# Kernel optimization log

Measured on AMD Instinct MI355X. Metric: run time of the kernel, lower is better.

## Reference

```python
import jax, jax.numpy as jnp
import numpy as np

N_NODES = 10000
N_EDGES = 160000
D = 256
L = 2
EPS = 1e-5


def setup_inputs() -> dict:
    key = jax.random.key(0)
    ks = jax.random.split(key, 12)
    s = 0.05  # weight init scale to keep activations tame
    return {
        "node_h": jax.random.normal(ks[0], (N_NODES, D), jnp.float32),
        "edge_h": jax.random.normal(ks[1], (N_EDGES, D), jnp.float32),
        "src": jax.random.randint(ks[2], (N_EDGES,), 0, N_NODES, jnp.int32),
        "dst": jax.random.randint(ks[3], (N_EDGES,), 0, N_NODES, jnp.int32),
        "Kw": jax.random.normal(ks[4], (L, 2 * D, D), jnp.float32) * s,
        "Kb": jnp.zeros((L, D), jnp.float32),
        "Vw": jax.random.normal(ks[5], (L, 2 * D, D), jnp.float32) * s,
        "Vb": jnp.zeros((L, D), jnp.float32),
        "Qw": jax.random.normal(ks[6], (L, D, D), jnp.float32) * s,
        "Qb": jnp.zeros((L, D), jnp.float32),
        "Ww": jax.random.normal(ks[7], (L, 2 * D, D), jnp.float32) * s,
        "Wb": jnp.zeros((L, D), jnp.float32),
        "Ew": jax.random.normal(ks[8], (L, 3 * D, D), jnp.float32) * s,
        "Eb": jnp.zeros((L, D), jnp.float32),
        "ln_g": jnp.ones((D,), jnp.float32),
        "ln_b": jnp.zeros((D,), jnp.float32),
    }


def _layernorm(x, g, b):
    mu = jnp.mean(x, axis=-1, keepdims=True)
    var = jnp.mean(jnp.square(x - mu), axis=-1, keepdims=True)
    return (x - mu) * jax.lax.rsqrt(var + EPS) * g + b


def _hypergraph_layer(h_n, h_e, src, dst, Kw, Kb, Vw, Vb, Qw, Qb, Ww, Wb, Ew, Eb):
    n = h_n.shape[0]
    src_h = h_n[src]                                   # [E, D] gather
    msg = jnp.concatenate([src_h * h_e, src_h], axis=1)  # [E, 2D]
    Q = h_n @ Qw + Qb                                  # [N, D]
    K = msg @ Kw + Kb                                  # [E, D]
    V = msg @ Vw + Vb                                  # [E, D]
    alpha = Q[dst] * K                                 # v_mul_e -> [E, D]
    # edge_softmax: per-destination-node, per-feature softmax over edges
    m = jax.ops.segment_max(alpha, dst, num_segments=n)
    e = jnp.exp(alpha - m[dst])
    z = jax.ops.segment_sum(e, dst, num_segments=n)
    a = e / z[dst]
    agg = jax.ops.segment_sum(a * V, dst, num_segments=n)  # sum aggregation [N, D]
    h_n_new = jnp.concatenate([agg, h_n], axis=1) @ Ww + Wb
    h_e_new = jnp.concatenate([h_n_new[src], h_n_new[dst], h_e], axis=1) @ Ew + Eb
    return h_n_new, h_e_new


def reference(node_h, edge_h, src, dst, Kw, Kb, Vw, Vb, Qw, Qb, Ww, Wb, Ew, Eb, ln_g, ln_b):
    h_n, h_e = node_h, edge_h
    for l in range(L):  # small fixed layer count
        h_n, h_e = _hypergraph_layer(h_n, h_e, src, dst,
                                     Kw[l], Kb[l], Vw[l], Vb[l], Qw[l], Qb[l],
                                     Ww[l], Wb[l], Ew[l], Eb[l])
        # relu -> layernorm; dropout is identity in eval mode
        h_n = _layernorm(jax.nn.relu(h_n), ln_g, ln_b)
        h_e = _layernorm(jax.nn.relu(h_e), ln_g, ln_b)
    return h_n, h_e
```

## Files before the change

kernel.cpp:

```cpp
#include <hip/hip_runtime.h>

#define NN 10000
#define NE 160000
#define DD 256
#define LEPS 1e-5f

typedef __attribute__((ext_vector_type(8))) short short8v;
typedef __attribute__((ext_vector_type(4))) float floatx4;
typedef unsigned short US;

static __device__ __forceinline__ US f2bf(float f){
  unsigned u = __builtin_bit_cast(unsigned, f);
  u += 0x7FFFu + ((u >> 16) & 1u);
  return (US)(u >> 16);
}
static __device__ __forceinline__ float bf2f(US s){
  unsigned u = ((unsigned)s) << 16;
  return __builtin_bit_cast(float, u);
}

__global__ void pack_k(const float* __restrict__ B, US* __restrict__ Bp, int Krows){
  int i = blockIdx.x * blockDim.x + threadIdx.x;
  int tot = (Krows >> 3) << 8;
  if (i >= tot) return;
  int kb = i >> 8, n = i & 255;
  union { US h[8]; uint4 q; } pk;
#pragma unroll
  for (int j = 0; j < 8; ++j) pk.h[j] = f2bf(B[(size_t)(kb*8 + j)*DD + n]);
  *(uint4*)(Bp + (size_t)i * 8) = pk.q;
}

template<int MODE, int LNM>
__global__ __launch_bounds__(256, 2)
void gemm_k(const float* __restrict__ p0, const float* __restrict__ p1,
            const int* __restrict__ idx0, const int* __restrict__ idx1,
            const US* __restrict__ Bp, const float* __restrict__ bias,
            const float* __restrict__ lg, const float* __restrict__ lb,
            float* __restrict__ Craw, float* __restrict__ Cln, int M, int K)
{
  __shared__ __align__(16) US Alds[64][40];
  __shared__ __align__(16) US Blds[4 * 256 * 8];
  __shared__ float S1[4][64], S2[4][64];
  const int tid  = threadIdx.x;
  const int lane = tid & 63;
  const int wav  = tid >> 6;
  const int bm   = blockIdx.x * 64;

  floatx4 acc[4][4];
#pragma unroll
  for (int i = 0; i < 4; ++i)
#pragma unroll
    for (int j = 0; j < 4; ++j) acc[i][j] = (floatx4){0.f,0.f,0.f,0.f};

  const int ar = tid >> 2;
  const int ak = (tid & 3) << 3;
  int grow = bm + ar; if (grow > M - 1) grow = M - 1;

  const float* rA = nullptr; const float* rB = nullptr; const float* rC = nullptr;
  if (MODE == 0) { rA = p0 + (size_t)grow * DD; }
  else if (MODE == 2) { rA = p0 + (size_t)grow * DD; rB = p1 + (size_t)grow * DD; }
  else { int s0 = idx0[grow], s1 = idx1[grow];
         rA = p0 + (size_t)s0 * DD; rB = p0 + (size_t)s1 * DD; rC = p1 + (size_t)grow * DD; }

  const int rq = lane >> 4;
  const int cl = lane & 15;

  for (int k0 = 0; k0 < K; k0 += 32) {
    const int kk = k0 + ak;
    float4 x0, x1;
    if (MODE == 0) {
      x0 = *(const float4*)(rA + kk); x1 = *(const float4*)(rA + kk + 4);
    } else if (MODE == 2) {
      const float* s = (kk < DD) ? (rA + kk) : (rB + kk - DD);
      x0 = *(const float4*)s; x1 = *(const float4*)(s + 4);
    } else {
      const float* s = (kk < DD) ? (rA + kk) : (kk < 2*DD ? (rB + kk - DD) : (rC + kk - 2*DD));
      x0 = *(const float4*)s; x1 = *(const float4*)(s + 4);
    }
    union { US h[8]; uint4 q; } pk;
    pk.h[0]=f2bf(x0.x); pk.h[1]=f2bf(x0.y); pk.h[2]=f2bf(x0.z); pk.h[3]=f2bf(x0.w);
    pk.h[4]=f2bf(x1.x); pk.h[5]=f2bf(x1.y); pk.h[6]=f2bf(x1.z); pk.h[7]=f2bf(x1.w);
    *(uint4*)&Alds[ar][ak] = pk.q;

    const uint4* bsrc = (const uint4*)(Bp + (size_t)(k0 >> 3) * 2048);
    uint4* bdst = (uint4*)Blds;
#pragma unroll
    for (int t = 0; t < 4; ++t) bdst[tid + t*256] = bsrc[tid + t*256];
    __syncthreads();

    short8v af[4], bfr[4];
#pragma unroll
    for (int i = 0; i < 4; ++i) af[i] = *(const short8v*)&Alds[i*16 + cl][rq*8];
#pragma unroll
    for (int j = 0; j < 4; ++j) bfr[j] = *(const short8v*)&Blds[(size_t)(rq*256 + wav*64 + j*16 + cl) * 8];
#pragma unroll
    for (int i = 0; i < 4; ++i)
#pragma unroll
      for (int j = 0; j < 4; ++j)
        acc[i][j] = __builtin_amdgcn_mfma_f32_16x16x32_bf16(af[i], bfr[j], acc[i][j], 0, 0, 0);
    __syncthreads();
  }

  if constexpr (LNM == 0) {
#pragma unroll
    for (int i = 0; i < 4; ++i)
#pragma unroll
      for (int r = 0; r < 4; ++r) {
        int gm = bm + i*16 + rq*4 + r;
        if (gm < M) {
#pragma unroll
          for (int j = 0; j < 4; ++j) {
            int n = wav*64 + j*16 + cl;
            Craw[(size_t)gm*DD + n] = acc[i][j][r] + bias[n];
          }
        }
      }
  } else {
#pragma unroll
    for (int i = 0; i < 4; ++i)
#pragma unroll
      for (int j = 0; j < 4; ++j) {
        int n = wav*64 + j*16 + cl;
        float bs = bias[n];
#pragma unroll
        for (int r = 0; r < 4; ++r) {
          int gm = bm + i*16 + rq*4 + r;
          float val = acc[i][j][r] + bs;
          if constexpr (LNM == 2) { if (gm < M) Craw[(size_t)gm*DD + n] = val; }
          acc[i][j][r] = fmaxf(val, 0.f);
        }
      }
#pragma unroll
    for (int i = 0; i < 4; ++i)
#pragma unroll
      for (int r = 0; r < 4; ++r) {
        float s1 = 0.f, s2 = 0.f;
#pragma unroll
        for (int j = 0; j < 4; ++j){ float v = acc[i][j][r]; s1 += v; s2 += v*v; }
#pragma unroll
        for (int o = 1; o < 16; o <<= 1){ s1 += __shfl_xor(s1, o, 64); s2 += __shfl_xor(s2, o, 64); }
        if (cl == 0){ S1[wav][i*16 + rq*4 + r] = s1; S2[wav][i*16 + rq*4 + r] = s2; }
      }
    __syncthreads();
#pragma unroll
    for (int i = 0; i < 4; ++i)
#pragma unroll
      for (int r = 0; r < 4; ++r) {
        int rr = i*16 + rq*4 + r;
        float t1 = S1[0][rr] + S1[1][rr] + S1[2][rr] + S1[3][rr];
        float t2 = S2[0][rr] + S2[1][rr] + S2[2][rr] + S2[3][rr];
        float mu = t1 * (1.f/256.f);
        float var = t2 * (1.f/256.f) - mu*mu;
        float rs = rsqrtf(fmaxf(var, 0.f) + LEPS);
        int gm = bm + i*16 + rq*4 + r;
        if (gm < M) {
#pragma unroll
          for (int j = 0; j < 4; ++j) {
            int n = wav*64 + j*16 + cl;
            Cln[(size_t)gm*DD + n] = (acc[i][j][r] - mu) * rs * lg[n] + lb[n];
          }
        }
      }
  }
}

__global__ __launch_bounds__(256, 2)
void gemm_kv_k(const float* __restrict__ p0, const float* __restrict__ p1,
               const int* __restrict__ idx0,
               const US* __restrict__ BpK, const US* __restrict__ BpV,
               const float* __restrict__ biasK, const float* __restrict__ biasV,
               const int* __restrict__ eperm,
               US* __restrict__ Km, US* __restrict__ Vm, int M, int K)
{
  __shared__ __align__(16) US Alds[64][40];
  __shared__ __align__(16) US BldsK[4 * 256 * 8];
  __shared__ __align__(16) US BldsV[4 * 256 * 8];
  const int tid  = threadIdx.x;
  const int lane = tid & 63;
  const int wav  = tid >> 6;
  const int bm   = blockIdx.x * 64;

  floatx4 accK[4][4], accV[4][4];
#pragma unroll
  for (int i = 0; i < 4; ++i)
#pragma unroll
    for (int j = 0; j < 4; ++j){ accK[i][j] = (floatx4){0.f,0.f,0.f,0.f}; accV[i][j] = (floatx4){0.f,0.f,0.f,0.f}; }

  const int ar = tid >> 2;
  const int ak = (tid & 3) << 3;
  int grow = bm + ar; if (grow > M - 1) grow = M - 1;
  int s = idx0[grow];
  const float* rA = p0 + (size_t)s * DD;
  const float* rB = p1 + (size_t)grow * DD;

  const int rq = lane >> 4;
  const int cl = lane & 15;

  for (int k0 = 0; k0 < K; k0 += 32) {
    const int kk = k0 + ak;
    float4 x0, x1;
    if (kk < DD) {
      x0 = *(const float4*)(rA + kk); x1 = *(const float4*)(rA + kk + 4);
      float4 m0 = *(const float4*)(rB + kk), m1 = *(const float4*)(rB + kk + 4);
      x0.x*=m0.x; x0.y*=m0.y; x0.z*=m0.z; x0.w*=m0.w;
      x1.x*=m1.x; x1.y*=m1.y; x1.z*=m1.z; x1.w*=m1.w;
    } else {
      x0 = *(const float4*)(rA + kk - DD); x1 = *(const float4*)(rA + kk - DD + 4);
    }
    union { US h[8]; uint4 q; } pk;
    pk.h[0]=f2bf(x0.x); pk.h[1]=f2bf(x0.y); pk.h[2]=f2bf(x0.z); pk.h[3]=f2bf(x0.w);
    pk.h[4]=f2bf(x1.x); pk.h[5]=f2bf(x1.y); pk.h[6]=f2bf(x1.z); pk.h[7]=f2bf(x1.w);
    *(uint4*)&Alds[ar][ak] = pk.q;

    const uint4* bsK = (const uint4*)(BpK + (size_t)(k0 >> 3) * 2048);
    const uint4* bsV = (const uint4*)(BpV + (size_t)(k0 >> 3) * 2048);
    uint4* bdK = (uint4*)BldsK; uint4* bdV = (uint4*)BldsV;
#pragma unroll
    for (int t = 0; t < 4; ++t){ bdK[tid + t*256] = bsK[tid + t*256]; bdV[tid + t*256] = bsV[tid + t*256]; }
    __syncthreads();

    short8v af[4], bK[4], bV[4];
#pragma unroll
    for (int i = 0; i < 4; ++i) af[i] = *(const short8v*)&Alds[i*16 + cl][rq*8];
#pragma unroll
    for (int j = 0; j < 4; ++j){
      size_t bi = (size_t)(rq*256 + wav*64 + j*16 + cl) * 8;
      bK[j] = *(const short8v*)&BldsK[bi];
      bV[j] = *(const short8v*)&BldsV[bi];
    }
#pragma unroll
    for (int i = 0; i < 4; ++i)
#pragma unroll
      for (int j = 0; j < 4; ++j){
        accK[i][j] = __builtin_amdgcn_mfma_f32_16x16x32_bf16(af[i], bK[j], accK[i][j], 0, 0, 0);
        accV[i][j] = __builtin_amdgcn_mfma_f32_16x16x32_bf16(af[i], bV[j], accV[i][j], 0, 0, 0);
      }
    __syncthreads();
  }

#pragma unroll
  for (int i = 0; i < 4; ++i)
#pragma unroll
    for (int r = 0; r < 4; ++r) {
      int gm = bm + i*16 + rq*4 + r;
      if (gm < M) {
        int pg = eperm[gm];
#pragma unroll
        for (int j = 0; j < 4; ++j) {
          int n = wav*64 + j*16 + cl;
          Km[(size_t)pg*DD + n] = f2bf(accK[i][j][r] + biasK[n]);
          Vm[(size_t)pg*DD + n] = f2bf(accV[i][j][r] + biasV[n]);
        }
      }
    }
}

__global__ void count_k(const int* __restrict__ dst, int* __restrict__ cnt, int e){
  int i = blockIdx.x * blockDim.x + threadIdx.x;
  if (i < e) atomicAdd(&cnt[dst[i]], 1);
}
__global__ void scan_k(const int* __restrict__ cnt, int* __restrict__ rp, int n){
  __shared__ int part[256];
  const int t = threadIdx.x;
  const int chunk = (n + 255) / 256;
  int lo = t * chunk, hi = lo + chunk; if (hi > n) hi = n; if (lo > n) lo = n;
  int s = 0;
  for (int i = lo; i < hi; ++i) s += cnt[i];
  part[t] = s; __syncthreads();
  if (t == 0){ int run = 0; for (int i = 0; i < 256; ++i){ int tmp = part[i]; part[i] = run; run += tmp; } rp[n] = run; }
  __syncthreads();
  int run = part[t];
  for (int i = lo; i < hi; ++i){ rp[i] = run; run += cnt[i]; }
}
__global__ void scatter_k(const int* __restrict__ dst, const int* __restrict__ rp,
                          int* __restrict__ pos, int* __restrict__ eperm, int e){
  int i = blockIdx.x * blockDim.x + threadIdx.x;
  if (i >= e) return;
  int d = dst[i];
  int p = atomicAdd(&pos[d], 1);
  eperm[i] = rp[d] + p;
}

__global__ __launch_bounds__(256)
void node_agg_k(const int* __restrict__ rp,
                const float* __restrict__ Q, const US* __restrict__ Km,
                const US* __restrict__ Vm, float* __restrict__ agg)
{
  int d = blockIdx.x, f = threadIdx.x;
  int beg = rp[d], end = rp[d + 1];
  float q = Q[(size_t)d * DD + f];
  float m = -3.0e38f, z = 0.f, s = 0.f;
  for (int i = beg; i < end; ++i){
    float a  = q * bf2f(Km[(size_t)i * DD + f]);
    float vv = bf2f(Vm[(size_t)i * DD + f]);
    float mn = fmaxf(m, a);
    float sc = __expf(m - mn);
    float w  = __expf(a - mn);
    z = z * sc + w;
    s = s * sc + w * vv;
    m = mn;
  }
  agg[(size_t)d * DD + f] = (z > 0.f) ? (s / z) : 0.f;
}

__global__ void sentinel_k(int hostbits, float* out){
  int code = 0;
  if (hostbits & 1) code = 1;
  else if (hostbits & 2) code = 2;
  else if (hostbits & 4) code = 3;
  else if (hostbits & 8) code = 4;
  if (code) out[0] = (float)code * 1.0e6f;
}

extern "C" void kernel_launch(void* const* d_in, const int* in_sizes, int n_in,
                              void* d_out, int out_size, void* d_ws, size_t ws_size,
                              hipStream_t stream) {
  const float* node_h = (const float*)d_in[0];
  const float* edge_h = (const float*)d_in[1];
  const int*   src    = (const int*)d_in[2];
  const int*   dst    = (const int*)d_in[3];
  const float* Kw = (const float*)d_in[4];  const float* Kb = (const float*)d_in[5];
  const float* Vw = (const float*)d_in[6];  const float* Vb = (const float*)d_in[7];
  const float* Qw = (const float*)d_in[8];  const float* Qb = (const float*)d_in[9];
  const float* Ww = (const float*)d_in[10]; const float* Wb = (const float*)d_in[11];
  const float* Ew = (const float*)d_in[12]; const float* Eb = (const float*)d_in[13];
  const float* ln_g = (const float*)d_in[14];
  const float* ln_b = (const float*)d_in[15];

  char* w = (char*)d_ws; size_t off = 0;
  auto alloc = [&](size_t bytes)->char* {
    char* p = w + off; off += (bytes + 255) & ~(size_t)255; return p;
  };
  float* Q      = (float*)alloc((size_t)NN * DD * 4);
  float* agg    = (float*)alloc((size_t)NN * DD * 4);
  float* hn_new = (float*)alloc((size_t)NN * DD * 4);
  float* hn_cur = (float*)alloc((size_t)NN * DD * 4);
  US*    Kmat   = (US*)alloc((size_t)NE * DD * 2);
  US*    Vmat   = (US*)alloc((size_t)NE * DD * 2);
  float* he_cur = (float*)alloc((size_t)NE * DD * 4);
  US* BpK = (US*)alloc((size_t)512 * DD * 2);
  US* BpV = (US*)alloc((size_t)512 * DD * 2);
  US* BpQ = (US*)alloc((size_t)256 * DD * 2);
  US* BpW = (US*)alloc((size_t)512 * DD * 2);
  US* BpE = (US*)alloc((size_t)768 * DD * 2);
  int* cnt   = (int*)alloc((size_t)NN * 4);
  int* rp    = (int*)alloc((size_t)(NN + 1) * 4);
  int* pos   = (int*)alloc((size_t)NN * 4);
  int* eperm = (int*)alloc((size_t)NE * 4);

  float* out_hn = (float*)d_out;
  float* out_he = out_hn + (size_t)NN * DD;

  int hostbits = 0;
  {
    static const int exp_sizes[16] = {NN*DD, NE*DD, NE, NE, 2*512*DD, 2*DD, 2*512*DD, 2*DD,
                                      2*DD*DD, 2*DD, 2*512*DD, 2*DD, 2*768*DD, 2*DD, DD, DD};
    if (n_in != 16) hostbits |= 2;
    else { for (int i = 0; i < 16; ++i) if (in_sizes[i] != exp_sizes[i]) hostbits |= 2; }
    if (out_size != NN*DD + NE*DD) hostbits |= 4;
    if (off > ws_size) hostbits |= 1;
  }
  if (hostbits) {
    sentinel_k<<<1, 1, 0, stream>>>(hostbits, out_hn);
    return;
  }

  hipMemsetAsync(cnt, 0, (size_t)NN * 4, stream);
  hipMemsetAsync(pos, 0, (size_t)NN * 4, stream);
  count_k<<<(NE + 255)/256, 256, 0, stream>>>(dst, cnt, NE);
  scan_k<<<1, 256, 0, stream>>>(cnt, rp, NN);
  scatter_k<<<(NE + 255)/256, 256, 0, stream>>>(dst, rp, pos, eperm, NE);

  const int gN = (NN + 63) / 64;
  const int gE = (NE + 63) / 64;

  for (int l = 0; l < 2; ++l) {
    const float* hn_in = l ? hn_cur : node_h;
    const float* he_in = l ? he_cur : edge_h;
    float* hn_out = l ? out_hn : hn_cur;
    float* he_out = l ? out_he : he_cur;

    pack_k<<<(512*DD/8 + 255)/256, 256, 0, stream>>>(Kw + (size_t)l*512*DD, BpK, 512);
    pack_k<<<(512*DD/8 + 255)/256, 256, 0, stream>>>(Vw + (size_t)l*512*DD, BpV, 512);
    pack_k<<<(256*DD/8 + 255)/256, 256, 0, stream>>>(Qw + (size_t)l*256*DD, BpQ, 256);
    pack_k<<<(512*DD/8 + 255)/256, 256, 0, stream>>>(Ww + (size_t)l*512*DD, BpW, 512);
    pack_k<<<(768*DD/8 + 255)/256, 256, 0, stream>>>(Ew + (size_t)l*768*DD, BpE, 768);

    gemm_k<0, 0><<<gN, 256, 0, stream>>>(hn_in, nullptr, nullptr, nullptr,
                                         BpQ, Qb + (size_t)l*DD, nullptr, nullptr,
                                         Q, nullptr, NN, 256);
    gemm_kv_k<<<gE, 256, 0, stream>>>(hn_in, he_in, src, BpK, BpV,
                                      Kb + (size_t)l*DD, Vb + (size_t)l*DD,
                                      eperm, Kmat, Vmat, NE, 512);
    node_agg_k<<<NN, 256, 0, stream>>>(rp, Q, Kmat, Vmat, agg);
    gemm_k<2, 2><<<gN, 256, 0, stream>>>(agg, hn_in, nullptr, nullptr,
                                         BpW, Wb + (size_t)l*DD, ln_g, ln_b,
                                         hn_new, hn_out, NN, 512);
    gemm_k<3, 1><<<gE, 256, 0, stream>>>(hn_new, he_in, src, dst,
                                         BpE, Eb + (size_t)l*DD, ln_g, ln_b,
                                         nullptr, he_out, NE, 768);
  }

  if (hipGetLastError() != hipSuccess) {
    sentinel_k<<<1, 1, 0, stream>>>(8, out_hn);
  }
}
```

Before: 907.7 us.

## Double-buffer GEMM tiles and stage B via global_load_lds

```diff
diff --git a/kernel.cpp b/kernel.cpp
--- a/kernel.cpp
+++ b/kernel.cpp
@@ -17,6 +17,10 @@
 static __device__ __forceinline__ float bf2f(US s){
   unsigned u = ((unsigned)s) << 16;
   return __builtin_bit_cast(float, u);
+}
+static __device__ __forceinline__ void gl_lds16(const void* g, void* l){
+  __builtin_amdgcn_global_load_lds((const __attribute__((address_space(1))) unsigned int*)g,
+                                   (__attribute__((address_space(3))) unsigned int*)l, 16, 0, 0);
 }
 
 __global__ void pack_k(const float* __restrict__ B, US* __restrict__ Bp, int Krows){
@@ -31,15 +35,15 @@
 }
 
 template<int MODE, int LNM>
-__global__ __launch_bounds__(256, 2)
+__global__ __launch_bounds__(256, 3)
 void gemm_k(const float* __restrict__ p0, const float* __restrict__ p1,
             const int* __restrict__ idx0, const int* __restrict__ idx1,
             const US* __restrict__ Bp, const float* __restrict__ bias,
             const float* __restrict__ lg, const float* __restrict__ lb,
             float* __restrict__ Craw, float* __restrict__ Cln, int M, int K)
 {
-  __shared__ __align__(16) US Alds[64][40];
-  __shared__ __align__(16) US Blds[4 * 256 * 8];
+  __shared__ __align__(16) US Alds[2][64][40];
+  __shared__ __align__(16) US Blds[2][8192];
   __shared__ float S1[4][64], S2[4][64];
   const int tid  = threadIdx.x;
   const int lane = tid & 63;
@@ -64,41 +68,49 @@
 
   const int rq = lane >> 4;
   const int cl = lane & 15;
-
-  for (int k0 = 0; k0 < K; k0 += 32) {
-    const int kk = k0 + ak;
-    float4 x0, x1;
-    if (MODE == 0) {
-      x0 = *(const float4*)(rA + kk); x1 = *(const float4*)(rA + kk + 4);
-    } else if (MODE == 2) {
-      const float* s = (kk < DD) ? (rA + kk) : (rB + kk - DD);
-      x0 = *(const float4*)s; x1 = *(const float4*)(s + 4);
-    } else {
-      const float* s = (kk < DD) ? (rA + kk) : (kk < 2*DD ? (rB + kk - DD) : (rC + kk - 2*DD));
-      x0 = *(const float4*)s; x1 = *(const float4*)(s + 4);
-    }
+  const int nsteps = K >> 5;
+
+  float4 f0, f1;
+  auto ldA = [&](int t){
+    int kk = t*32 + ak;
+    const float* s;
+    if (MODE == 0) s = rA + kk;
+    else if (MODE == 2) s = (kk < DD) ? (rA + kk) : (rB + kk - DD);
+    else s = (kk < DD) ? (rA + kk) : (kk < 2*DD ? (rB + kk - DD) : (rC + kk - 2*DD));
+    f0 = *(const float4*)s; f1 = *(const float4*)(s + 4);
+  };
+  auto packA = [&](int buf){
     union { US h[8]; uint4 q; } pk;
-    pk.h[0]=f2bf(x0.x); pk.h[1]=f2bf(x0.y); pk.h[2]=f2bf(x0.z); pk.h[3]=f2bf(x0.w);
-    pk.h[4]=f2bf(x1.x); pk.h[5]=f2bf(x1.y); pk.h[6]=f2bf(x1.z); pk.h[7]=f2bf(x1.w);
-    *(uint4*)&Alds[ar][ak] = pk.q;
-
-    const uint4* bsrc = (const uint4*)(Bp + (size_t)(k0 >> 3) * 2048);
-    uint4* bdst = (uint4*)Blds;
-#pragma unroll
-    for (int t = 0; t < 4; ++t) bdst[tid + t*256] = bsrc[tid + t*256];
-    __syncthreads();
-
+    pk.h[0]=f2bf(f0.x); pk.h[1]=f2bf(f0.y); pk.h[2]=f2bf(f0.z); pk.h[3]=f2bf(f0.w);
+    pk.h[4]=f2bf(f1.x); pk.h[5]=f2bf(f1.y); pk.h[6]=f2bf(f1.z); pk.h[7]=f2bf(f1.w);
+    *(uint4*)&Alds[buf][ar][ak] = pk.q;
+  };
+  auto stageB = [&](int t, int buf){
+    const US* bs = Bp + (size_t)(t*4) * 2048;
+#pragma unroll
+    for (int u = 0; u < 4; ++u)
+      gl_lds16(bs + (size_t)(tid + u*256)*8, &Blds[buf][(size_t)(tid + u*256)*8]);
+  };
+
+  ldA(0); stageB(0, 0); packA(0);
+  __syncthreads();
+
+  int cur = 0;
+  for (int t = 0; t < nsteps; ++t) {
+    if (t + 1 < nsteps) { stageB(t + 1, cur ^ 1); ldA(t + 1); }
     short8v af[4], bfr[4];
 #pragma unroll
-    for (int i = 0; i < 4; ++i) af[i] = *(const short8v*)&Alds[i*16 + cl][rq*8];
-#pragma unroll
-    for (int j = 0; j < 4; ++j) bfr[j] = *(const short8v*)&Blds[(size_t)(rq*256 + wav*64 + j*16 + cl) * 8];
+    for (int i = 0; i < 4; ++i) af[i] = *(const short8v*)&Alds[cur][i*16 + cl][rq*8];
+#pragma unroll
+    for (int j = 0; j < 4; ++j) bfr[j] = *(const short8v*)&Blds[cur][(size_t)(rq*256 + wav*64 + j*16 + cl) * 8];
 #pragma unroll
     for (int i = 0; i < 4; ++i)
 #pragma unroll
       for (int j = 0; j < 4; ++j)
         acc[i][j] = __builtin_amdgcn_mfma_f32_16x16x32_bf16(af[i], bfr[j], acc[i][j], 0, 0, 0);
+    if (t + 1 < nsteps) packA(cur ^ 1);
     __syncthreads();
+    cur ^= 1;
   }
 
   if constexpr (LNM == 0) {
@@ -172,9 +184,8 @@
                const int* __restrict__ eperm,
                US* __restrict__ Km, US* __restrict__ Vm, int M, int K)
 {
-  __shared__ __align__(16) US Alds[64][40];
-  __shared__ __align__(16) US BldsK[4 * 256 * 8];
-  __shared__ __align__(16) US BldsV[4 * 256 * 8];
+  __shared__ __align__(16) US Alds[2][64][40];
+  __shared__ __align__(16) US Blds[2][2][8192];
   const int tid  = threadIdx.x;
   const int lane = tid & 63;
   const int wav  = tid >> 6;
@@ -195,47 +206,65 @@
 
   const int rq = lane >> 4;
   const int cl = lane & 15;
-
-  for (int k0 = 0; k0 < K; k0 += 32) {
-    const int kk = k0 + ak;
-    float4 x0, x1;
-    if (kk < DD) {
-      x0 = *(const float4*)(rA + kk); x1 = *(const float4*)(rA + kk + 4);
-      float4 m0 = *(const float4*)(rB + kk), m1 = *(const float4*)(rB + kk + 4);
-      x0.x*=m0.x; x0.y*=m0.y; x0.z*=m0.z; x0.w*=m0.w;
-      x1.x*=m1.x; x1.y*=m1.y; x1.z*=m1.z; x1.w*=m1.w;
+  const int nsteps = K >> 5;
+
+  float4 f0, f1, g0, g1;
+  auto ldA = [&](int t){
+    int kk = t*32 + ak;
+    if (kk < DD){
+      f0 = *(const float4*)(rA + kk); f1 = *(const float4*)(rA + kk + 4);
+      g0 = *(const float4*)(rB + kk); g1 = *(const float4*)(rB + kk + 4);
     } else {
-      x0 = *(const float4*)(rA + kk - DD); x1 = *(const float4*)(rA + kk - DD + 4);
+      f0 = *(const float4*)(rA + kk - DD); f1 = *(const float4*)(rA + kk - DD + 4);
+    }
+  };
+  auto packA = [&](int t, int buf){
+    int kk = t*32 + ak;
+    float4 x0 = f0, x1 = f1;
+    if (kk < DD){
+      x0.x*=g0.x; x0.y*=g0.y; x0.z*=g0.z; x0.w*=g0.w;
+      x1.x*=g1.x; x1.y*=g1.y; x1.z*=g1.z; x1.w*=g1.w;
     }
     union { US h[8]; uint4 q; } pk;
     pk.h[0]=f2bf(x0.x); pk.h[1]=f2bf(x0.y); pk.h[2]=f2bf(x0.z); pk.h[3]=f2bf(x0.w);
     pk.h[4]=f2bf(x1.x); pk.h[5]=f2bf(x1.y); pk.h[6]=f2bf(x1.z); pk.h[7]=f2bf(x1.w);
-    *(uint4*)&Alds[ar][ak] = pk.q;
-
-    const uint4* bsK = (const uint4*)(BpK + (size_t)(k0 >> 3) * 2048);
-    const uint4* bsV = (const uint4*)(BpV + (size_t)(k0 >> 3) * 2048);
-    uint4* bdK = (uint4*)BldsK; uint4* bdV = (uint4*)BldsV;
-#pragma unroll
-    for (int t = 0; t < 4; ++t){ bdK[tid + t*256] = bsK[tid + t*256]; bdV[tid + t*256] = bsV[tid + t*256]; }
-    __syncthreads();
-
-    short8v af[4], bK[4], bV[4];
-#pragma unroll
-    for (int i = 0; i < 4; ++i) af[i] = *(const short8v*)&Alds[i*16 + cl][rq*8];
+    *(uint4*)&Alds[buf][ar][ak] = pk.q;
+  };
+  auto stageB = [&](int t, int buf){
+    const US* bK = BpK + (size_t)(t*4) * 2048;
+    const US* bV = BpV + (size_t)(t*4) * 2048;
+#pragma unroll
+    for (int u = 0; u < 4; ++u){
+      gl_lds16(bK + (size_t)(tid + u*256)*8, &Blds[buf][0][(size_t)(tid + u*256)*8]);
+      gl_lds16(bV + (size_t)(tid + u*256)*8, &Blds[buf][1][(size_t)(tid + u*256)*8]);
+    }
+  };
+
+  ldA(0); stageB(0, 0); packA(0, 0);
+  __syncthreads();
+
+  int cur = 0;
+  for (int t = 0; t < nsteps; ++t) {
+    if (t + 1 < nsteps) { stageB(t + 1, cur ^ 1); ldA(t + 1); }
+    short8v af[4], bK4[4], bV4[4];
+#pragma unroll
+    for (int i = 0; i < 4; ++i) af[i] = *(const short8v*)&Alds[cur][i*16 + cl][rq*8];
 #pragma unroll
     for (int j = 0; j < 4; ++j){
       size_t bi = (size_t)(rq*256 + wav*64 + j*16 + cl) * 8;
-      bK[j] = *(const short8v*)&BldsK[bi];
-      bV[j] = *(const short8v*)&BldsV[bi];
+      bK4[j] = *(const short8v*)&Blds[cur][0][bi];
+      bV4[j] = *(const short8v*)&Blds[cur][1][bi];
     }
 #pragma unroll
     for (int i = 0; i < 4; ++i)
 #pragma unroll
       for (int j = 0; j < 4; ++j){
-        accK[i][j] = __builtin_amdgcn_mfma_f32_16x16x32_bf16(af[i], bK[j], accK[i][j], 0, 0, 0);
-        accV[i][j] = __builtin_amdgcn_mfma_f32_16x16x32_bf16(af[i], bV[j], accV[i][j], 0, 0, 0);
-      }
+        accK[i][j] = __builtin_amdgcn_mfma_f32_16x16x32_bf16(af[i], bK4[j], accK[i][j], 0, 0, 0);
+        accV[i][j] = __builtin_amdgcn_mfma_f32_16x16x32_bf16(af[i], bV4[j], accV[i][j], 0, 0, 0);
+      }
+    if (t + 1 < nsteps) packA(t + 1, cur ^ 1);
     __syncthreads();
+    cur ^= 1;
   }
 
 #pragma unroll
```

Result: slower. 1.018 ms (+12.2%).

## Precompute node-level GEMM parts to shrink per-edge K, V and E GEMMs

Applied to the files above, without the earlier changes.

```diff
diff --git a/kernel.cpp b/kernel.cpp
--- a/kernel.cpp
+++ b/kernel.cpp
@@ -19,27 +19,113 @@
   return __builtin_bit_cast(float, u);
 }
 
-__global__ void pack_k(const float* __restrict__ B, US* __restrict__ Bp, int Krows){
-  int i = blockIdx.x * blockDim.x + threadIdx.x;
-  int tot = (Krows >> 3) << 8;
-  if (i >= tot) return;
-  int kb = i >> 8, n = i & 255;
+#define AOFF_Q  0
+#define AOFF_K1 (32*2048)
+#define AOFF_K2 (64*2048)
+#define AOFF_V1 (96*2048)
+#define AOFF_V2 (128*2048)
+#define AOFF_W  (160*2048)
+#define AOFF_E1 (224*2048)
+#define AOFF_E2 (256*2048)
+#define AOFF_E3 (288*2048)
+__global__ void pack_all_k(const float* __restrict__ Qw, const float* __restrict__ Kw,
+                           const float* __restrict__ Vw, const float* __restrict__ Ww,
+                           const float* __restrict__ Ew, US* __restrict__ arena){
+  int i = blockIdx.x * 256 + threadIdx.x;
+  int g = i >> 8, n = i & 255;
+  const float* src; int row0;
+  if      (g <  32){ src = Qw; row0 = g*8; }
+  else if (g <  64){ src = Kw; row0 = (g-32)*8; }
+  else if (g <  96){ src = Kw; row0 = 256 + (g-64)*8; }
+  else if (g < 128){ src = Vw; row0 = (g-96)*8; }
+  else if (g < 160){ src = Vw; row0 = 256 + (g-128)*8; }
+  else if (g < 224){ src = Ww; row0 = (g-160)*8; }
+  else if (g < 256){ src = Ew; row0 = (g-224)*8; }
+  else if (g < 288){ src = Ew; row0 = 256 + (g-256)*8; }
+  else             { src = Ew; row0 = 512 + (g-288)*8; }
   union { US h[8]; uint4 q; } pk;
 #pragma unroll
-  for (int j = 0; j < 8; ++j) pk.h[j] = f2bf(B[(size_t)(kb*8 + j)*DD + n]);
-  *(uint4*)(Bp + (size_t)i * 8) = pk.q;
-}
-
-template<int MODE, int LNM>
+  for (int j = 0; j < 8; ++j) pk.h[j] = f2bf(src[(size_t)(row0 + j)*DD + n]);
+  *(uint4*)(arena + (size_t)g*2048 + n*8) = pk.q;
+}
+
+struct Tri { const US* bp; const float* bias; float* out; };
 __global__ __launch_bounds__(256, 2)
-void gemm_k(const float* __restrict__ p0, const float* __restrict__ p1,
-            const int* __restrict__ idx0, const int* __restrict__ idx1,
-            const US* __restrict__ Bp, const float* __restrict__ bias,
-            const float* __restrict__ lg, const float* __restrict__ lb,
-            float* __restrict__ Craw, float* __restrict__ Cln, int M, int K)
+void gemm_nmulti_k(const float* __restrict__ p0, Tri t0, Tri t1, Tri t2, int M)
+{
+  Tri t = (blockIdx.y == 0) ? t0 : (blockIdx.y == 1 ? t1 : t2);
+  __shared__ __align__(16) US Alds[64][40];
+  __shared__ __align__(16) US Blds[8192];
+  const int tid  = threadIdx.x;
+  const int lane = tid & 63;
+  const int wav  = tid >> 6;
+  const int bm   = blockIdx.x * 64;
+
+  floatx4 acc[4][4];
+#pragma unroll
+  for (int i = 0; i < 4; ++i)
+#pragma unroll
+    for (int j = 0; j < 4; ++j) acc[i][j] = (floatx4){0.f,0.f,0.f,0.f};
+
+  const int ar = tid >> 2;
+  const int ak = (tid & 3) << 3;
+  int grow = bm + ar; if (grow > M - 1) grow = M - 1;
+  const float* rA = p0 + (size_t)grow * DD;
+  const int rq = lane >> 4;
+  const int cl = lane & 15;
+
+  for (int k0 = 0; k0 < 256; k0 += 32) {
+    const int kk = k0 + ak;
+    float4 x0 = *(const float4*)(rA + kk);
+    float4 x1 = *(const float4*)(rA + kk + 4);
+    union { US h[8]; uint4 q; } pk;
+    pk.h[0]=f2bf(x0.x); pk.h[1]=f2bf(x0.y); pk.h[2]=f2bf(x0.z); pk.h[3]=f2bf(x0.w);
+    pk.h[4]=f2bf(x1.x); pk.h[5]=f2bf(x1.y); pk.h[6]=f2bf(x1.z); pk.h[7]=f2bf(x1.w);
+    *(uint4*)&Alds[ar][ak] = pk.q;
+
+    const uint4* bsrc = (const uint4*)(t.bp + (size_t)(k0 >> 3) * 2048);
+    uint4* bdst = (uint4*)Blds;
+#pragma unroll
+    for (int u = 0; u < 4; ++u) bdst[tid + u*256] = bsrc[tid + u*256];
+    __syncthreads();
+
+    short8v af[4], bfr[4];
+#pragma unroll
+    for (int i = 0; i < 4; ++i) af[i] = *(const short8v*)&Alds[i*16 + cl][rq*8];
+#pragma unroll
+    for (int j = 0; j < 4; ++j) bfr[j] = *(const short8v*)&Blds[(size_t)(rq*256 + wav*64 + j*16 + cl) * 8];
+#pragma unroll
+    for (int i = 0; i < 4; ++i)
+#pragma unroll
+      for (int j = 0; j < 4; ++j)
+        acc[i][j] = __builtin_amdgcn_mfma_f32_16x16x32_bf16(af[i], bfr[j], acc[i][j], 0, 0, 0);
+    __syncthreads();
+  }
+
+#pragma unroll
+  for (int i = 0; i < 4; ++i)
+#pragma unroll
+    for (int r = 0; r < 4; ++r) {
+      int gm = bm + i*16 + rq*4 + r;
+      if (gm < M) {
+#pragma unroll
+        for (int j = 0; j < 4; ++j) {
+          int n = wav*64 + j*16 + cl;
+          float b = t.bias ? t.bias[n] : 0.f;
+          t.out[(size_t)gm*DD + n] = acc[i][j][r] + b;
+        }
+      }
+    }
+}
+
+__global__ __launch_bounds__(256, 2)
+void gemm_w_k(const float* __restrict__ p0, const float* __restrict__ p1,
+              const US* __restrict__ Bp, const float* __restrict__ bias,
+              const float* __restrict__ lg, const float* __restrict__ lb,
+              float* __restrict__ Craw, float* __restrict__ Cln, int M)
 {
   __shared__ __align__(16) US Alds[64][40];
-  __shared__ __align__(16) US Blds[4 * 256 * 8];
+  __shared__ __align__(16) US Blds[8192];
   __shared__ float S1[4][64], S2[4][64];
   const int tid  = threadIdx.x;
   const int lane = tid & 63;
@@ -55,28 +141,16 @@
   const int ar = tid >> 2;
   const int ak = (tid & 3) << 3;
   int grow = bm + ar; if (grow > M - 1) grow = M - 1;
-
-  const float* rA = nullptr; const float* rB = nullptr; const float* rC = nullptr;
-  if (MODE == 0) { rA = p0 + (size_t)grow * DD; }
-  else if (MODE == 2) { rA = p0 + (size_t)grow * DD; rB = p1 + (size_t)grow * DD; }
-  else { int s0 = idx0[grow], s1 = idx1[grow];
-         rA = p0 + (size_t)s0 * DD; rB = p0 + (size_t)s1 * DD; rC = p1 + (size_t)grow * DD; }
-
+  const float* rA = p0 + (size_t)grow * DD;
+  const float* rB = p1 + (size_t)grow * DD;
   const int rq = lane >> 4;
   const int cl = lane & 15;
 
-  for (int k0 = 0; k0 < K; k0 += 32) {
+  for (int k0 = 0; k0 < 512; k0 += 32) {
     const int kk = k0 + ak;
-    float4 x0, x1;
-    if (MODE == 0) {
-      x0 = *(const float4*)(rA + kk); x1 = *(const float4*)(rA + kk + 4);
-    } else if (MODE == 2) {
-      const float* s = (kk < DD) ? (rA + kk) : (rB + kk - DD);
-      x0 = *(const float4*)s; x1 = *(const float4*)(s + 4);
-    } else {
-      const float* s = (kk < DD) ? (rA + kk) : (kk < 2*DD ? (rB + kk - DD) : (rC + kk - 2*DD));
-      x0 = *(const float4*)s; x1 = *(const float4*)(s + 4);
-    }
+    const float* s = (kk < DD) ? (rA + kk) : (rB + kk - DD);
+    float4 x0 = *(const float4*)s;
+    float4 x1 = *(const float4*)(s + 4);
     union { US h[8]; uint4 q; } pk;
     pk.h[0]=f2bf(x0.x); pk.h[1]=f2bf(x0.y); pk.h[2]=f2bf(x0.z); pk.h[3]=f2bf(x0.w);
     pk.h[4]=f2bf(x1.x); pk.h[5]=f2bf(x1.y); pk.h[6]=f2bf(x1.z); pk.h[7]=f2bf(x1.w);
@@ -85,7 +159,7 @@
     const uint4* bsrc = (const uint4*)(Bp + (size_t)(k0 >> 3) * 2048);
     uint4* bdst = (uint4*)Blds;
 #pragma unroll
-    for (int t = 0; t < 4; ++t) bdst[tid + t*256] = bsrc[tid + t*256];
+    for (int u = 0; u < 4; ++u) bdst[tid + u*256] = bsrc[tid + u*256];
     __syncthreads();
 
     short8v af[4], bfr[4];
@@ -101,80 +175,64 @@
     __syncthreads();
   }
 
-  if constexpr (LNM == 0) {
-#pragma unroll
-    for (int i = 0; i < 4; ++i)
+#pragma unroll
+  for (int i = 0; i < 4; ++i)
+#pragma unroll
+    for (int j = 0; j < 4; ++j) {
+      int n = wav*64 + j*16 + cl;
+      float bs = bias[n];
 #pragma unroll
       for (int r = 0; r < 4; ++r) {
         int gm = bm + i*16 + rq*4 + r;
-        if (gm < M) {
-#pragma unroll
-          for (int j = 0; j < 4; ++j) {
-            int n = wav*64 + j*16 + cl;
-            Craw[(size_t)gm*DD + n] = acc[i][j][r] + bias[n];
-          }
+        float val = acc[i][j][r] + bs;
+        if (gm < M) Craw[(size_t)gm*DD + n] = val;
+        acc[i][j][r] = fmaxf(val, 0.f);
+      }
+    }
+#pragma unroll
+  for (int i = 0; i < 4; ++i)
+#pragma unroll
+    for (int r = 0; r < 4; ++r) {
+      float s1 = 0.f, s2 = 0.f;
+#pragma unroll
+      for (int j = 0; j < 4; ++j){ float v = acc[i][j][r]; s1 += v; s2 += v*v; }
+#pragma unroll
+      for (int o = 1; o < 16; o <<= 1){ s1 += __shfl_xor(s1, o, 64); s2 += __shfl_xor(s2, o, 64); }
+      if (cl == 0){ S1[wav][i*16 + rq*4 + r] = s1; S2[wav][i*16 + rq*4 + r] = s2; }
+    }
+  __syncthreads();
+#pragma unroll
+  for (int i = 0; i < 4; ++i)
+#pragma unroll
+    for (int r = 0; r < 4; ++r) {
+      int rr = i*16 + rq*4 + r;
+      float t1 = S1[0][rr] + S1[1][rr] + S1[2][rr] + S1[3][rr];
+      float t2 = S2[0][rr] + S2[1][rr] + S2[2][rr] + S2[3][rr];
+      float mu = t1 * (1.f/256.f);
+      float var = t2 * (1.f/256.f) - mu*mu;
+      float rs = rsqrtf(fmaxf(var, 0.f) + LEPS);
+      int gm = bm + i*16 + rq*4 + r;
+      if (gm < M) {
+#pragma unroll
+        for (int j = 0; j < 4; ++j) {
+          int n = wav*64 + j*16 + cl;
+          Cln[(size_t)gm*DD + n] = (acc[i][j][r] - mu) * rs * lg[n] + lb[n];
         }
       }
-  } else {
-#pragma unroll
-    for (int i = 0; i < 4; ++i)
-#pragma unroll
-      for (int j = 0; j < 4; ++j) {
-        int n = wav*64 + j*16 + cl;
-        float bs = bias[n];
-#pragma unroll
-        for (int r = 0; r < 4; ++r) {
-          int gm = bm + i*16 + rq*4 + r;
-          float val = acc[i][j][r] + bs;
-          if constexpr (LNM == 2) { if (gm < M) Craw[(size_t)gm*DD + n] = val; }
-          acc[i][j][r] = fmaxf(val, 0.f);
-        }
-      }
-#pragma unroll
-    for (int i = 0; i < 4; ++i)
-#pragma unroll
-      for (int r = 0; r < 4; ++r) {
-        float s1 = 0.f, s2 = 0.f;
-#pragma unroll
-        for (int j = 0; j < 4; ++j){ float v = acc[i][j][r]; s1 += v; s2 += v*v; }
-#pragma unroll
-        for (int o = 1; o < 16; o <<= 1){ s1 += __shfl_xor(s1, o, 64); s2 += __shfl_xor(s2, o, 64); }
-        if (cl == 0){ S1[wav][i*16 + rq*4 + r] = s1; S2[wav][i*16 + rq*4 + r] = s2; }
-      }
-    __syncthreads();
-#pragma unroll
-    for (int i = 0; i < 4; ++i)
-#pragma unroll
-      for (int r = 0; r < 4; ++r) {
-        int rr = i*16 + rq*4 + r;
-        float t1 = S1[0][rr] + S1[1][rr] + S1[2][rr] + S1[3][rr];
-        float t2 = S2[0][rr] + S2[1][rr] + S2[2][rr] + S2[3][rr];
-        float mu = t1 * (1.f/256.f);
-        float var = t2 * (1.f/256.f) - mu*mu;
-        float rs = rsqrtf(fmaxf(var, 0.f) + LEPS);
-        int gm = bm + i*16 + rq*4 + r;
-        if (gm < M) {
-#pragma unroll
-          for (int j = 0; j < 4; ++j) {
-            int n = wav*64 + j*16 + cl;
-            Cln[(size_t)gm*DD + n] = (acc[i][j][r] - mu) * rs * lg[n] + lb[n];
-          }
-        }
-      }
-  }
+    }
 }
 
 __global__ __launch_bounds__(256, 2)
-void gemm_kv_k(const float* __restrict__ p0, const float* __restrict__ p1,
-               const int* __restrict__ idx0,
-               const US* __restrict__ BpK, const US* __restrict__ BpV,
-               const float* __restrict__ biasK, const float* __restrict__ biasV,
-               const int* __restrict__ eperm,
-               US* __restrict__ Km, US* __restrict__ Vm, int M, int K)
+void gemm_kve_k(const float* __restrict__ p0, const float* __restrict__ p1,
+                const int* __restrict__ srcI,
+                const US* __restrict__ BpK, const US* __restrict__ BpV,
+                const float* __restrict__ KN, const float* __restrict__ VN,
+                const int* __restrict__ eperm,
+                US* __restrict__ Km, US* __restrict__ Vm, int M)
 {
   __shared__ __align__(16) US Alds[64][40];
-  __shared__ __align__(16) US BldsK[4 * 256 * 8];
-  __shared__ __align__(16) US BldsV[4 * 256 * 8];
+  __shared__ __align__(16) US BldsK[8192];
+  __shared__ __align__(16) US BldsV[8192];
   const int tid  = threadIdx.x;
   const int lane = tid & 63;
   const int wav  = tid >> 6;
@@ -189,24 +247,20 @@
   const int ar = tid >> 2;
   const int ak = (tid & 3) << 3;
   int grow = bm + ar; if (grow > M - 1) grow = M - 1;
-  int s = idx0[grow];
+  int s = srcI[grow];
   const float* rA = p0 + (size_t)s * DD;
   const float* rB = p1 + (size_t)grow * DD;
-
   const int rq = lane >> 4;
   const int cl = lane & 15;
 
-  for (int k0 = 0; k0 < K; k0 += 32) {
+  for (int k0 = 0; k0 < 256; k0 += 32) {
     const int kk = k0 + ak;
-    float4 x0, x1;
-    if (kk < DD) {
-      x0 = *(const float4*)(rA + kk); x1 = *(const float4*)(rA + kk + 4);
-      float4 m0 = *(const float4*)(rB + kk), m1 = *(const float4*)(rB + kk + 4);
-      x0.x*=m0.x; x0.y*=m0.y; x0.z*=m0.z; x0.w*=m0.w;
-      x1.x*=m1.x; x1.y*=m1.y; x1.z*=m1.z; x1.w*=m1.w;
-    } else {
-      x0 = *(const float4*)(rA + kk - DD); x1 = *(const float4*)(rA + kk - DD + 4);
-    }
+    float4 x0 = *(const float4*)(rA + kk);
+    float4 x1 = *(const float4*)(rA + kk + 4);
+    float4 m0 = *(const float4*)(rB + kk);
+    float4 m1 = *(const float4*)(rB + kk + 4);
+    x0.x*=m0.x; x0.y*=m0.y; x0.z*=m0.z; x0.w*=m0.w;
+    x1.x*=m1.x; x1.y*=m1.y; x1.z*=m1.z; x1.w*=m1.w;
     union { US h[8]; uint4 q; } pk;
     pk.h[0]=f2bf(x0.x); pk.h[1]=f2bf(x0.y); pk.h[2]=f2bf(x0.z); pk.h[3]=f2bf(x0.w);
     pk.h[4]=f2bf(x1.x); pk.h[5]=f2bf(x1.y); pk.h[6]=f2bf(x1.z); pk.h[7]=f2bf(x1.w);
@@ -216,24 +270,24 @@
     const uint4* bsV = (const uint4*)(BpV + (size_t)(k0 >> 3) * 2048);
     uint4* bdK = (uint4*)BldsK; uint4* bdV = (uint4*)BldsV;
 #pragma unroll
-    for (int t = 0; t < 4; ++t){ bdK[tid + t*256] = bsK[tid + t*256]; bdV[tid + t*256] = bsV[tid + t*256]; }
-    __syncthreads();
-
-    short8v af[4], bK[4], bV[4];
+    for (int u = 0; u < 4; ++u){ bdK[tid + u*256] = bsK[tid + u*256]; bdV[tid + u*256] = bsV[tid + u*256]; }
+    __syncthreads();
+
+    short8v af[4], bK4[4], bV4[4];
 #pragma unroll
     for (int i = 0; i < 4; ++i) af[i] = *(const short8v*)&Alds[i*16 + cl][rq*8];
 #pragma unroll
     for (int j = 0; j < 4; ++j){
       size_t bi = (size_t)(rq*256 + wav*64 + j*16 + cl) * 8;
-      bK[j] = *(const short8v*)&BldsK[bi];
-      bV[j] = *(const short8v*)&BldsV[bi];
+      bK4[j] = *(const short8v*)&BldsK[bi];
+      bV4[j] = *(const short8v*)&BldsV[bi];
     }
 #pragma unroll
     for (int i = 0; i < 4; ++i)
 #pragma unroll
       for (int j = 0; j < 4; ++j){
-        accK[i][j] = __builtin_amdgcn_mfma_f32_16x16x32_bf16(af[i], bK[j], accK[i][j], 0, 0, 0);
-        accV[i][j] = __builtin_amdgcn_mfma_f32_16x16x32_bf16(af[i], bV[j], accV[i][j], 0, 0, 0);
+        accK[i][j] = __builtin_amdgcn_mfma_f32_16x16x32_bf16(af[i], bK4[j], accK[i][j], 0, 0, 0);
+        accV[i][j] = __builtin_amdgcn_mfma_f32_16x16x32_bf16(af[i], bV4[j], accV[i][j], 0, 0, 0);
       }
     __syncthreads();
   }
@@ -245,11 +299,118 @@
       int gm = bm + i*16 + rq*4 + r;
       if (gm < M) {
         int pg = eperm[gm];
+        int sg = srcI[gm];
+        const float* kn = KN + (size_t)sg * DD;
+        const float* vn = VN + (size_t)sg * DD;
 #pragma unroll
         for (int j = 0; j < 4; ++j) {
           int n = wav*64 + j*16 + cl;
-          Km[(size_t)pg*DD + n] = f2bf(accK[i][j][r] + biasK[n]);
-          Vm[(size_t)pg*DD + n] = f2bf(accV[i][j][r] + biasV[n]);
+          Km[(size_t)pg*DD + n] = f2bf(accK[i][j][r] + kn[n]);
+          Vm[(size_t)pg*DD + n] = f2bf(accV[i][j][r] + vn[n]);
+        }
+      }
+    }
+}
+
+__global__ __launch_bounds__(256, 2)
+void gemm_e_k(const float* __restrict__ he, const int* __restrict__ srcI,
+              const int* __restrict__ dstI, const US* __restrict__ Bp,
+              const float* __restrict__ EN1, const float* __restrict__ EN2,
+              const float* __restrict__ lg, const float* __restrict__ lb,
+              float* __restrict__ Cln, int M)
+{
+  __shared__ __align__(16) US Alds[64][40];
+  __shared__ __align__(16) US Blds[8192];
+  __shared__ float S1[4][64], S2[4][64];
+  const int tid  = threadIdx.x;
+  const int lane = tid & 63;
+  const int wav  = tid >> 6;
+  const int bm   = blockIdx.x * 64;
+
+  floatx4 acc[4][4];
+#pragma unroll
+  for (int i = 0; i < 4; ++i)
+#pragma unroll
+    for (int j = 0; j < 4; ++j) acc[i][j] = (floatx4){0.f,0.f,0.f,0.f};
+
+  const int ar = tid >> 2;
+  const int ak = (tid & 3) << 3;
+  int grow = bm + ar; if (grow > M - 1) grow = M - 1;
+  const float* rA = he + (size_t)grow * DD;
+  const int rq = lane >> 4;
+  const int cl = lane & 15;
+
+  for (int k0 = 0; k0 < 256; k0 += 32) {
+    const int kk = k0 + ak;
+    float4 x0 = *(const float4*)(rA + kk);
+    float4 x1 = *(const float4*)(rA + kk + 4);
+    union { US h[8]; uint4 q; } pk;
+    pk.h[0]=f2bf(x0.x); pk.h[1]=f2bf(x0.y); pk.h[2]=f2bf(x0.z); pk.h[3]=f2bf(x0.w);
+    pk.h[4]=f2bf(x1.x); pk.h[5]=f2bf(x1.y); pk.h[6]=f2bf(x1.z); pk.h[7]=f2bf(x1.w);
+    *(uint4*)&Alds[ar][ak] = pk.q;
+
+    const uint4* bsrc = (const uint4*)(Bp + (size_t)(k0 >> 3) * 2048);
+    uint4* bdst = (uint4*)Blds;
+#pragma unroll
+    for (int u = 0; u < 4; ++u) bdst[tid + u*256] = bsrc[tid + u*256];
+    __syncthreads();
+
+    short8v af[4], bfr[4];
+#pragma unroll
+    for (int i = 0; i < 4; ++i) af[i] = *(const short8v*)&Alds[i*16 + cl][rq*8];
+#pragma unroll
+    for (int j = 0; j < 4; ++j) bfr[j] = *(const short8v*)&Blds[(size_t)(rq*256 + wav*64 + j*16 + cl) * 8];
+#pragma unroll
+    for (int i = 0; i < 4; ++i)
+#pragma unroll
+      for (int j = 0; j < 4; ++j)
+        acc[i][j] = __builtin_amdgcn_mfma_f32_16x16x32_bf16(af[i], bfr[j], acc[i][j], 0, 0, 0);
+    __syncthreads();
+  }
+
+#pragma unroll
+  for (int i = 0; i < 4; ++i)
+#pragma unroll
+    for (int r = 0; r < 4; ++r) {
+      int gm = bm + i*16 + rq*4 + r;
+      int gmc = (gm < M) ? gm : (M - 1);
+      const float* e1 = EN1 + (size_t)srcI[gmc] * DD;
+      const float* e2 = EN2 + (size_t)dstI[gmc] * DD;
+#pragma unroll
+      for (int j = 0; j < 4; ++j) {
+        int n = wav*64 + j*16 + cl;
+        float val = acc[i][j][r] + e1[n] + e2[n];
+        acc[i][j][r] = fmaxf(val, 0.f);
+      }
+    }
+#pragma unroll
+  for (int i = 0; i < 4; ++i)
+#pragma unroll
+    for (int r = 0; r < 4; ++r) {
+      float s1 = 0.f, s2 = 0.f;
+#pragma unroll
+      for (int j = 0; j < 4; ++j){ float v = acc[i][j][r]; s1 += v; s2 += v*v; }
+#pragma unroll
+      for (int o = 1; o < 16; o <<= 1){ s1 += __shfl_xor(s1, o, 64); s2 += __shfl_xor(s2, o, 64); }
+      if (cl == 0){ S1[wav][i*16 + rq*4 + r] = s1; S2[wav][i*16 + rq*4 + r] = s2; }
+    }
+  __syncthreads();
+#pragma unroll
+  for (int i = 0; i < 4; ++i)
+#pragma unroll
+    for (int r = 0; r < 4; ++r) {
+      int rr = i*16 + rq*4 + r;
+      float t1 = S1[0][rr] + S1[1][rr] + S1[2][rr] + S1[3][rr];
+      float t2 = S2[0][rr] + S2[1][rr] + S2[2][rr] + S2[3][rr];
+      float mu = t1 * (1.f/256.f);
+      float var = t2 * (1.f/256.f) - mu*mu;
+      float rs = rsqrtf(fmaxf(var, 0.f) + LEPS);
+      int gm = bm + i*16 + rq*4 + r;
+      if (gm < M) {
+#pragma unroll
+        for (int j = 0; j < 4; ++j) {
+          int n = wav*64 + j*16 + cl;
+          Cln[(size_t)gm*DD + n] = (acc[i][j][r] - mu) * rs * lg[n] + lb[n];
         }
       }
     }
@@ -335,14 +496,14 @@
   float* agg    = (float*)alloc((size_t)NN * DD * 4);
   float* hn_new = (float*)alloc((size_t)NN * DD * 4);
   float* hn_cur = (float*)alloc((size_t)NN * DD * 4);
+  float* KN     = (float*)alloc((size_t)NN * DD * 4);
+  float* VN     = (float*)alloc((size_t)NN * DD * 4);
+  float* EN1    = (float*)alloc((size_t)NN * DD * 4);
+  float* EN2    = (float*)alloc((size_t)NN * DD * 4);
   US*    Kmat   = (US*)alloc((size_t)NE * DD * 2);
   US*    Vmat   = (US*)alloc((size_t)NE * DD * 2);
   float* he_cur = (float*)alloc((size_t)NE * DD * 4);
-  US* BpK = (US*)alloc((size_t)512 * DD * 2);
-  US* BpV = (US*)alloc((size_t)512 * DD * 2);
-  US* BpQ = (US*)alloc((size_t)256 * DD * 2);
-  US* BpW = (US*)alloc((size_t)512 * DD * 2);
-  US* BpE = (US*)alloc((size_t)768 * DD * 2);
+  US*    arena  = (US*)alloc((size_t)320 * 2048 * 2);
   int* cnt   = (int*)alloc((size_t)NN * 4);
   int* rp    = (int*)alloc((size_t)(NN + 1) * 4);
   int* pos   = (int*)alloc((size_t)NN * 4);
@@ -380,25 +541,29 @@
     float* hn_out = l ? out_hn : hn_cur;
     float* he_out = l ? out_he : he_cur;
 
-    pack_k<<<(512*DD/8 + 255)/256, 256, 0, stream>>>(Kw + (size_t)l*512*DD, BpK, 512);
-    pack_k<<<(512*DD/8 + 255)/256, 256, 0, stream>>>(Vw + (size_t)l*512*DD, BpV, 512);
-    pack_k<<<(256*DD/8 + 255)/256, 256, 0, stream>>>(Qw + (size_t)l*256*DD, BpQ, 256);
-    pack_k<<<(512*DD/8 + 255)/256, 256, 0, stream>>>(Ww + (size_t)l*512*DD, BpW, 512);
-    pack_k<<<(768*DD/8 + 255)/256, 256, 0, stream>>>(Ew + (size_t)l*768*DD, BpE, 768);
-
-    gemm_k<0, 0><<<gN, 256, 0, stream>>>(hn_in, nullptr, nullptr, nullptr,
-                                         BpQ, Qb + (size_t)l*DD, nullptr, nullptr,
-                                         Q, nullptr, NN, 256);
-    gemm_kv_k<<<gE, 256, 0, stream>>>(hn_in, he_in, src, BpK, BpV,
-                                      Kb + (size_t)l*DD, Vb + (size_t)l*DD,
-                                      eperm, Kmat, Vmat, NE, 512);
+    pack_all_k<<<320, 256, 0, stream>>>(Qw + (size_t)l*256*DD, Kw + (size_t)l*512*DD,
+                                        Vw + (size_t)l*512*DD, Ww + (size_t)l*512*DD,
+                                        Ew + (size_t)l*768*DD, arena);
+
+    {
+      Tri tQ{arena + AOFF_Q,  Qb + (size_t)l*DD, Q};
+      Tri tK{arena + AOFF_K2, Kb + (size_t)l*DD, KN};
+      Tri tV{arena + AOFF_V2, Vb + (size_t)l*DD, VN};
+      gemm_nmulti_k<<<dim3(gN, 3), 256, 0, stream>>>(hn_in, tQ, tK, tV, NN);
+    }
+    gemm_kve_k<<<gE, 256, 0, stream>>>(hn_in, he_in, src,
+                                       arena + AOFF_K1, arena + AOFF_V1,
+                                       KN, VN, eperm, Kmat, Vmat, NE);
     node_agg_k<<<NN, 256, 0, stream>>>(rp, Q, Kmat, Vmat, agg);
-    gemm_k<2, 2><<<gN, 256, 0, stream>>>(agg, hn_in, nullptr, nullptr,
-                                         BpW, Wb + (size_t)l*DD, ln_g, ln_b,
-                                         hn_new, hn_out, NN, 512);
-    gemm_k<3, 1><<<gE, 256, 0, stream>>>(hn_new, he_in, src, dst,
-                                         BpE, Eb + (size_t)l*DD, ln_g, ln_b,
-                                         nullptr, he_out, NE, 768);
+    gemm_w_k<<<gN, 256, 0, stream>>>(agg, hn_in, arena + AOFF_W, Wb + (size_t)l*DD,
+                                     ln_g, ln_b, hn_new, hn_out, NN);
+    {
+      Tri t1{arena + AOFF_E1, Eb + (size_t)l*DD, EN1};
+      Tri t2{arena + AOFF_E2, nullptr, EN2};
+      gemm_nmulti_k<<<dim3(gN, 2), 256, 0, stream>>>(hn_new, t1, t2, t2, NN);
+    }
+    gemm_e_k<<<gE, 256, 0, stream>>>(he_in, src, dst, arena + AOFF_E3,
+                                     EN1, EN2, ln_g, ln_b, he_out, NE);
   }
 
   if (hipGetLastError() != hipSuccess) {
```

Result: no change. 899.6 us (-0.9%).
